# Optimization experiments

Hardware: AMD Instinct MI355X
Metric: run time of the kernel (lower is better)

## Reference

```python
import jax, jax.numpy as jnp
import numpy as np

B, T, D, H, DK, FF, V, L = 2, 1024, 768, 12, 64, 3072, 50257, 12


def setup_inputs() -> dict:
    key = jax.random.key(0)
    ks = jax.random.split(key, 9)
    s = 0.02  # matches nn.init.normal_(std=0.02)
    rn = lambda k, sh: jax.random.normal(k, sh, jnp.float32) * s
    return {
        "x": jax.random.randint(ks[0], (B, T), 0, V),
        "tok_emb": rn(ks[1], (V, D)),
        "pos_emb": rn(ks[2], (T, D)),
        "Wq": rn(ks[3], (L, D, D)), "bq": jnp.zeros((L, D), jnp.float32),
        "Wk": rn(ks[4], (L, D, D)), "bk": jnp.zeros((L, D), jnp.float32),
        "Wv": rn(ks[5], (L, D, D)), "bv": jnp.zeros((L, D), jnp.float32),
        "Wo": rn(ks[6], (L, D, D)), "bo": jnp.zeros((L, D), jnp.float32),
        "ln1_g": jnp.ones((L, D), jnp.float32), "ln1_b": jnp.zeros((L, D), jnp.float32),
        "ln2_g": jnp.ones((L, D), jnp.float32), "ln2_b": jnp.zeros((L, D), jnp.float32),
        "W1": rn(ks[7], (L, D, FF)), "b1": jnp.zeros((L, FF), jnp.float32),
        "W2": rn(ks[8], (L, FF, D)), "b2": jnp.zeros((L, D), jnp.float32),
        "lnf_g": jnp.ones((D,), jnp.float32), "lnf_b": jnp.zeros((D,), jnp.float32),
    }


def _ln(x, g, b, eps=1e-5):
    m = jnp.mean(x, axis=-1, keepdims=True)
    v = jnp.var(x, axis=-1, keepdims=True)  # biased var, like torch LayerNorm
    return (x - m) * jax.lax.rsqrt(v + eps) * g + b


def _forward(x, tok_emb, pos_emb, Wq, bq, Wk, bk, Wv, bv, Wo, bo,
             ln1_g, ln1_b, ln2_g, ln2_b, W1, b1, W2, b2, lnf_g, lnf_b):
    Bsz, Tn = x.shape
    h = tok_emb[x] + pos_emb[:Tn][None]  # [B,T,D]
    causal = jnp.tril(jnp.ones((Tn, Tn), dtype=bool))  # True = keep
    scale = 1.0 / np.sqrt(DK)

    def block(h, p):
        wq, bq_, wk, bk_, wv, bv_, wo, bo_, g1, be1, g2, be2, w1, bf1, w2, bf2 = p
        x2 = _ln(h, g1, be1)
        q = (x2 @ wq + bq_).reshape(Bsz, Tn, H, DK)
        k = (x2 @ wk + bk_).reshape(Bsz, Tn, H, DK)
        v = (x2 @ wv + bv_).reshape(Bsz, Tn, H, DK)
        scores = jnp.einsum("bqhd,bkhd->bhqk", q, k) * scale
        scores = jnp.where(causal, scores, -jnp.inf)
        attn = jax.nn.softmax(scores, axis=-1)  # dropout is identity in eval
        ctx = jnp.einsum("bhqk,bkhd->bqhd", attn, v).reshape(Bsz, Tn, D)
        h = h + ctx @ wo + bo_
        x2 = _ln(h, g2, be2)
        ff = jax.nn.gelu(x2 @ w1 + bf1, approximate=False) @ w2 + bf2  # exact GELU like F.gelu
        return h + ff, None

    params = (Wq, bq, Wk, bk, Wv, bv, Wo, bo, ln1_g, ln1_b, ln2_g, ln2_b, W1, b1, W2, b2)
    h, _ = jax.lax.scan(block, h, params)
    h = _ln(h, lnf_g, lnf_b)
    return h @ tok_emb.T  # tied lm_head, [B,T,V]


def reference(x, tok_emb, pos_emb, Wq, bq, Wk, bk, Wv, bv, Wo, bo,
              ln1_g, ln1_b, ln2_g, ln2_b, W1, b1, W2, b2, lnf_g, lnf_b):
    return _forward(x, tok_emb, pos_emb, Wq, bq, Wk, bk, Wv, bv, Wo, bo,
                    ln1_g, ln1_b, ln2_g, ln2_b, W1, b1, W2, b2, lnf_g, lnf_b)
```

## Files before the change

### kernel.cpp

```cpp
#include <hip/hip_runtime.h>
#include <cmath>

#define DI __device__ __forceinline__

typedef unsigned short u16;
typedef __bf16 bf16x8 __attribute__((ext_vector_type(8)));
typedef float f32x4 __attribute__((ext_vector_type(4)));

static constexpr int Bsz = 2, T = 1024, D = 768, H = 12, FF = 3072, V = 50257, L = 12;
static constexpr int M = Bsz * T;

DI u16 f2bf(float f) {
  unsigned u = __float_as_uint(f);
  u = (u + 0x7fffu + ((u >> 16) & 1u)) >> 16;
  return (u16)u;
}
DI float bf2f(u16 h) { return __uint_as_float(((unsigned)h) << 16); }

DI void gload_lds16(const void* g, void* l) {
  __builtin_amdgcn_global_load_lds((const __attribute__((address_space(1))) void*)g,
                                   (__attribute__((address_space(3))) void*)l, 16, 0, 0);
}

__launch_bounds__(256)
__global__ void transpose_cvt(const float* __restrict__ src, u16* __restrict__ dst, int R, int C) {
  __shared__ float tile[32][33];
  const int tx = threadIdx.x, ty = threadIdx.y;
  const int c0 = blockIdx.x * 32, r0 = blockIdx.y * 32;
  src += (size_t)blockIdx.z * R * C;
  dst += (size_t)blockIdx.z * R * C;
#pragma unroll
  for (int i = 0; i < 4; ++i)
    tile[ty + i * 8][tx] = src[(size_t)(r0 + ty + i * 8) * C + c0 + tx];
  __syncthreads();
#pragma unroll
  for (int i = 0; i < 4; ++i)
    dst[(size_t)(c0 + ty + i * 8) * R + r0 + tx] = f2bf(tile[tx][ty + i * 8]);
}

__global__ void convert_bf16(const float* __restrict__ src, u16* __restrict__ dst, long n4) {
  long i = (long)blockIdx.x * blockDim.x + threadIdx.x;
  long stride = (long)gridDim.x * blockDim.x;
  for (; i < n4; i += stride) {
    float4 f = ((const float4*)src)[i];
    ushort4 o;
    o.x = f2bf(f.x); o.y = f2bf(f.y); o.z = f2bf(f.z); o.w = f2bf(f.w);
    ((ushort4*)dst)[i] = o;
  }
}

__launch_bounds__(256)
__global__ void embed_kernel(const int* __restrict__ x, const float* __restrict__ tok,
                             const float* __restrict__ pos, float* __restrict__ h) {
  const int row = blockIdx.x, t = threadIdx.x;
  const int tt = row % T;
  const int id = x[row];
  float* o = h + (size_t)row * D;
  const float* te = tok + (size_t)id * D;
  const float* pe = pos + (size_t)tt * D;
  o[t] = te[t] + pe[t];
  o[t + 256] = te[t + 256] + pe[t + 256];
  o[t + 512] = te[t + 512] + pe[t + 512];
}

__launch_bounds__(256)
__global__ void layernorm_kernel(const float* __restrict__ in, const float* __restrict__ gw,
                                 const float* __restrict__ bw, u16* __restrict__ out) {
  const int row = blockIdx.x, t = threadIdx.x;
  const int lane = t & 63, wid = t >> 6;
  const float* x = in + (size_t)row * D;
  float v0 = x[t], v1 = x[t + 256], v2 = x[t + 512];
  float sum = v0 + v1 + v2;
  float sq = v0 * v0 + v1 * v1 + v2 * v2;
  for (int off = 1; off < 64; off <<= 1) {
    sum += __shfl_xor(sum, off);
    sq += __shfl_xor(sq, off);
  }
  __shared__ float ps[4], pq[4];
  if (lane == 0) { ps[wid] = sum; pq[wid] = sq; }
  __syncthreads();
  sum = ps[0] + ps[1] + ps[2] + ps[3];
  sq = pq[0] + pq[1] + pq[2] + pq[3];
  const float mean = sum * (1.0f / D);
  const float var = sq * (1.0f / D) - mean * mean;
  const float rstd = rsqrtf(var + 1e-5f);
  u16* o = out + (size_t)row * D;
  o[t] = f2bf((v0 - mean) * rstd * gw[t] + bw[t]);
  o[t + 256] = f2bf((v1 - mean) * rstd * gw[t + 256] + bw[t + 256]);
  o[t + 512] = f2bf((v2 - mean) * rstd * gw[t + 512] + bw[t + 512]);
}

template <int EPI, int BM, int BN, int BK>
DI void gemm_core(const u16* __restrict__ A, const u16* __restrict__ Bt,
                  const float* bias, float* outF, u16* outH, const float* resid,
                  int N, int K) {
  __shared__ u16 sA[BM * BK];
  __shared__ u16 sB[BN * BK];
  constexpr int FM = BM / 32, FN = BN / 32;
  constexpr int CPR = BK / 8;
  constexpr int KS = BK / 32;
  const int t = threadIdx.x;
  const int lane = t & 63, wid = t >> 6;
  const int m0 = blockIdx.x * BM, n0 = blockIdx.y * BN;

  f32x4 acc[FM][FN] = {};
  const int wr = (wid >> 1) * (BM / 2), wc = (wid & 1) * (BN / 2);
  const int rsel = lane & 15, ksel = lane >> 4;

  for (int k0 = 0; k0 < K; k0 += BK) {
#pragma unroll
    for (int i = 0; i < 2; ++i) {
      int c = t + i * 256;
      int row = c / CPR, ch = c % CPR;
      int g = ch ^ (row & (CPR - 1));
      gload_lds16(A + (size_t)(m0 + row) * K + k0 + g * 8, &sA[c * 8]);
    }
#pragma unroll
    for (int i = 0; i < 2; ++i) {
      int c = t + i * 256;
      int row = c / CPR, ch = c % CPR;
      int g = ch ^ (row & (CPR - 1));
      int nr = n0 + row;
      if (nr >= N) nr = N - 1;
      gload_lds16(Bt + (size_t)nr * K + k0 + g * 8, &sB[c * 8]);
    }
    __syncthreads();
#pragma unroll
    for (int ks = 0; ks < KS; ++ks) {
      bf16x8 af[FM], bfr[FN];
#pragma unroll
      for (int m = 0; m < FM; ++m) {
        int row = wr + m * 16 + rsel;
        int ch = (ksel + 4 * ks) ^ (row & (CPR - 1));
        af[m] = *(const bf16x8*)&sA[row * BK + ch * 8];
      }
#pragma unroll
      for (int n = 0; n < FN; ++n) {
        int row = wc + n * 16 + rsel;
        int ch = (ksel + 4 * ks) ^ (row & (CPR - 1));
        bfr[n] = *(const bf16x8*)&sB[row * BK + ch * 8];
      }
#pragma unroll
      for (int m = 0; m < FM; ++m)
#pragma unroll
        for (int n = 0; n < FN; ++n)
          acc[m][n] = __builtin_amdgcn_mfma_f32_16x16x32_bf16(af[m], bfr[n], acc[m][n], 0, 0, 0);
    }
    __syncthreads();
  }

  const int rq = lane >> 4;
#pragma unroll
  for (int m = 0; m < FM; ++m) {
#pragma unroll
    for (int n = 0; n < FN; ++n) {
      const int col = n0 + wc + n * 16 + rsel;
      if (col >= N) continue;
      const float bv = bias ? bias[col] : 0.0f;
#pragma unroll
      for (int i = 0; i < 4; ++i) {
        const int row = m0 + wr + m * 16 + rq * 4 + i;
        float v = acc[m][n][i] + bv;
        const size_t idx = (size_t)row * N + col;
        if (EPI == 0) {
          outH[idx] = f2bf(v);
        } else if (EPI == 1) {
          float ge = 0.5f * v * (1.0f + erff(v * 0.70710678118f));
          outH[idx] = f2bf(ge);
        } else if (EPI == 2) {
          outF[idx] = resid[idx] + v;
        } else {
          outF[idx] = v;
        }
      }
    }
  }
}

__launch_bounds__(256) __global__ void gemm_qkv(const u16* __restrict__ A, const u16* __restrict__ Bt,
                                                const float* b0, const float* b1, const float* b2,
                                                u16* out, long zsB, long zsOut) {
  const int z = blockIdx.z;
  gemm_core<0, 64, 64, 64>(A, Bt + (size_t)z * zsB, z == 0 ? b0 : (z == 1 ? b1 : b2),
                           nullptr, out + (size_t)z * zsOut, nullptr, D, D);
}
__launch_bounds__(256) __global__ void gemm_proj(const u16* __restrict__ A, const u16* __restrict__ Bt,
                                                 const float* bias, float* h) {
  gemm_core<2, 64, 64, 64>(A, Bt, bias, h, nullptr, h, D, D);
}
__launch_bounds__(256) __global__ void gemm_ff1(const u16* __restrict__ A, const u16* __restrict__ Bt,
                                                const float* bias, u16* out) {
  gemm_core<1, 128, 128, 32>(A, Bt, bias, nullptr, out, nullptr, FF, D);
}
__launch_bounds__(256) __global__ void gemm_ff2(const u16* __restrict__ A, const u16* __restrict__ Bt,
                                                const float* bias, float* h) {
  gemm_core<2, 64, 64, 64>(A, Bt, bias, h, nullptr, h, D, FF);
}
__launch_bounds__(256) __global__ void gemm_lm(const u16* __restrict__ A, const u16* __restrict__ Bt,
                                               float* out) {
  gemm_core<3, 128, 128, 32>(A, Bt, nullptr, out, nullptr, nullptr, V, D);
}

__launch_bounds__(256)
__global__ void attn_mfma(const u16* __restrict__ qbuf, const u16* __restrict__ kbuf,
                          const u16* __restrict__ vbuf, u16* __restrict__ ctx) {
  __shared__ u16 sK[64 * 64];
  __shared__ u16 sVT[64 * 72];
  __shared__ u16 sP[4][16 * 72];
  const int t = threadIdx.x, lane = t & 63, wid = t >> 6;
  const int l15 = lane & 15, g = lane >> 4;
  const int q0 = blockIdx.x * 64;
  const int bh = blockIdx.y;
  const int b = bh / H, hh = bh % H;
  const size_t rowbase = (size_t)b * T;
  u16* sPw = &sP[wid][0];

  const size_t qoff = (rowbase + q0 + wid * 16 + l15) * D + hh * 64 + g * 8;
  bf16x8 aQ0 = *(const bf16x8*)&qbuf[qoff];
  bf16x8 aQ1 = *(const bf16x8*)&qbuf[qoff + 32];

  float mr[4] = {-INFINITY, -INFINITY, -INFINITY, -INFINITY};
  float lr[4] = {0.f, 0.f, 0.f, 0.f};
  f32x4 o[4] = {};
  const int nt = blockIdx.x + 1;

  for (int kt = 0; kt < nt; ++kt) {
    __syncthreads();
#pragma unroll
    for (int i = 0; i < 2; ++i) {
      int c = t + i * 256;
      int row = c >> 3, ch = c & 7;
      gload_lds16(kbuf + (rowbase + kt * 64 + row) * D + hh * 64 + (size_t)(ch ^ (row & 7)) * 8,
                  &sK[c * 8]);
    }
#pragma unroll
    for (int i = 0; i < 2; ++i) {
      int key = t & 63, d0 = (t >> 6) * 8 + i * 32;
      bf16x8 v8 = *(const bf16x8*)&vbuf[(rowbase + kt * 64 + key) * D + hh * 64 + d0];
#pragma unroll
      for (int j = 0; j < 8; ++j) sVT[(d0 + j) * 72 + key] = ((u16*)&v8)[j];
    }
    __syncthreads();

    f32x4 s[4];
#pragma unroll
    for (int f = 0; f < 4; ++f) {
      const int krow = f * 16 + l15;
      bf16x8 bk0 = *(const bf16x8*)&sK[krow * 64 + ((g ^ (krow & 7)) * 8)];
      bf16x8 bk1 = *(const bf16x8*)&sK[krow * 64 + (((g + 4) ^ (krow & 7)) * 8)];
      f32x4 z = {};
      z = __builtin_amdgcn_mfma_f32_16x16x32_bf16(aQ0, bk0, z, 0, 0, 0);
      s[f] = __builtin_amdgcn_mfma_f32_16x16x32_bf16(aQ1, bk1, z, 0, 0, 0);
    }

    float p[4][4], scl[4];
#pragma unroll
    for (int i = 0; i < 4; ++i) {
      const int qrow = q0 + wid * 16 + g * 4 + i;
      const int kb = kt * 64 + l15;
      float v0 = (kb <= qrow) ? s[0][i] * 0.125f : -INFINITY;
      float v1 = (kb + 16 <= qrow) ? s[1][i] * 0.125f : -INFINITY;
      float v2 = (kb + 32 <= qrow) ? s[2][i] * 0.125f : -INFINITY;
      float v3 = (kb + 48 <= qrow) ? s[3][i] * 0.125f : -INFINITY;
      float mt = fmaxf(fmaxf(v0, v1), fmaxf(v2, v3));
#pragma unroll
      for (int off = 1; off < 16; off <<= 1) mt = fmaxf(mt, __shfl_xor(mt, off));
      const float mn = fmaxf(mr[i], mt);
      const float sc = __expf(mr[i] - mn);
      p[0][i] = __expf(v0 - mn); p[1][i] = __expf(v1 - mn);
      p[2][i] = __expf(v2 - mn); p[3][i] = __expf(v3 - mn);
      float rs = p[0][i] + p[1][i] + p[2][i] + p[3][i];
#pragma unroll
      for (int off = 1; off < 16; off <<= 1) rs += __shfl_xor(rs, off);
      lr[i] = lr[i] * sc + rs;
      mr[i] = mn;
      scl[i] = sc;
    }
#pragma unroll
    for (int n = 0; n < 4; ++n) {
      o[n][0] *= scl[0]; o[n][1] *= scl[1]; o[n][2] *= scl[2]; o[n][3] *= scl[3];
    }
#pragma unroll
    for (int f = 0; f < 4; ++f)
#pragma unroll
      for (int i = 0; i < 4; ++i)
        sPw[(g * 4 + i) * 72 + f * 16 + l15] = f2bf(p[f][i]);

#pragma unroll
    for (int kb = 0; kb < 2; ++kb) {
      bf16x8 pa = *(const bf16x8*)&sPw[l15 * 72 + kb * 32 + g * 8];
#pragma unroll
      for (int n = 0; n < 4; ++n) {
        bf16x8 bv = *(const bf16x8*)&sVT[(n * 16 + l15) * 72 + kb * 32 + g * 8];
        o[n] = __builtin_amdgcn_mfma_f32_16x16x32_bf16(pa, bv, o[n], 0, 0, 0);
      }
    }
  }

  float inv[4] = {1.0f / lr[0], 1.0f / lr[1], 1.0f / lr[2], 1.0f / lr[3]};
#pragma unroll
  for (int n = 0; n < 4; ++n)
#pragma unroll
    for (int i = 0; i < 4; ++i)
      ctx[(rowbase + q0 + wid * 16 + g * 4 + i) * D + hh * 64 + n * 16 + l15] =
          f2bf(o[n][i] * inv[i]);
}

extern "C" void kernel_launch(void* const* d_in, const int* in_sizes, int n_in,
                              void* d_out, int out_size, void* d_ws, size_t ws_size,
                              hipStream_t stream) {
  (void)in_sizes; (void)n_in; (void)out_size;
  const int* x = (const int*)d_in[0];
  const float* tok = (const float*)d_in[1];
  const float* pos = (const float*)d_in[2];
  const float* Wq = (const float*)d_in[3];
  const float* bq = (const float*)d_in[4];
  const float* Wk = (const float*)d_in[5];
  const float* bk = (const float*)d_in[6];
  const float* Wv = (const float*)d_in[7];
  const float* bv = (const float*)d_in[8];
  const float* Wo = (const float*)d_in[9];
  const float* bo = (const float*)d_in[10];
  const float* ln1_g = (const float*)d_in[11];
  const float* ln1_b = (const float*)d_in[12];
  const float* ln2_g = (const float*)d_in[13];
  const float* ln2_b = (const float*)d_in[14];
  const float* W1 = (const float*)d_in[15];
  const float* b1 = (const float*)d_in[16];
  const float* W2 = (const float*)d_in[17];
  const float* b2 = (const float*)d_in[18];
  const float* lnf_g = (const float*)d_in[19];
  const float* lnf_b = (const float*)d_in[20];

  char* ws = (char*)d_ws;
  size_t off = 0;
  auto alloc = [&](size_t bytes) {
    void* p = ws + off;
    off += (bytes + 255) & ~(size_t)255;
    return p;
  };
  u16* wqkvT = (u16*)alloc((size_t)3 * L * D * D * 2);
  u16* woT   = (u16*)alloc((size_t)L * D * D * 2);
  u16* w1T   = (u16*)alloc((size_t)L * D * FF * 2);
  u16* w2T   = (u16*)alloc((size_t)L * FF * D * 2);
  u16* tokT  = (u16*)alloc((size_t)V * D * 2);
  float* h   = (float*)alloc((size_t)M * D * 4);
  u16* x2    = (u16*)alloc((size_t)M * D * 2);
  u16* qkv   = (u16*)alloc((size_t)3 * M * D * 2);
  u16* ctx   = (u16*)alloc((size_t)M * D * 2);
  u16* ffb   = (u16*)alloc((size_t)M * FF * 2);
  u16* hf    = (u16*)alloc((size_t)M * D * 2);
  if (off > ws_size) return;

  const dim3 tb(32, 8);
  transpose_cvt<<<dim3(D / 32, D / 32, L), tb, 0, stream>>>(Wq, wqkvT + (size_t)0 * L * D * D, D, D);
  transpose_cvt<<<dim3(D / 32, D / 32, L), tb, 0, stream>>>(Wk, wqkvT + (size_t)1 * L * D * D, D, D);
  transpose_cvt<<<dim3(D / 32, D / 32, L), tb, 0, stream>>>(Wv, wqkvT + (size_t)2 * L * D * D, D, D);
  transpose_cvt<<<dim3(D / 32, D / 32, L), tb, 0, stream>>>(Wo, woT, D, D);
  transpose_cvt<<<dim3(FF / 32, D / 32, L), tb, 0, stream>>>(W1, w1T, D, FF);
  transpose_cvt<<<dim3(D / 32, FF / 32, L), tb, 0, stream>>>(W2, w2T, FF, D);
  convert_bf16<<<2048, 256, 0, stream>>>(tok, tokT, (long)V * D / 4);

  embed_kernel<<<M, 256, 0, stream>>>(x, tok, pos, h);

  for (int l = 0; l < L; ++l) {
    layernorm_kernel<<<M, 256, 0, stream>>>(h, ln1_g + (size_t)l * D, ln1_b + (size_t)l * D, x2);
    gemm_qkv<<<dim3(M / 64, D / 64, 3), 256, 0, stream>>>(
        x2, wqkvT + (size_t)l * D * D, bq + (size_t)l * D, bk + (size_t)l * D, bv + (size_t)l * D,
        qkv, (long)L * D * D, (long)M * D);
    attn_mfma<<<dim3(T / 64, Bsz * H), 256, 0, stream>>>(qkv, qkv + (size_t)M * D,
                                                         qkv + (size_t)2 * M * D, ctx);
    gemm_proj<<<dim3(M / 64, D / 64), 256, 0, stream>>>(ctx, woT + (size_t)l * D * D,
                                                        bo + (size_t)l * D, h);
    layernorm_kernel<<<M, 256, 0, stream>>>(h, ln2_g + (size_t)l * D, ln2_b + (size_t)l * D, x2);
    gemm_ff1<<<dim3(M / 128, FF / 128), 256, 0, stream>>>(x2, w1T + (size_t)l * D * FF,
                                                          b1 + (size_t)l * FF, ffb);
    gemm_ff2<<<dim3(M / 64, D / 64), 256, 0, stream>>>(ffb, w2T + (size_t)l * FF * D,
                                                       b2 + (size_t)l * D, h);
  }

  layernorm_kernel<<<M, 256, 0, stream>>>(h, lnf_g, lnf_b, hf);
  gemm_lm<<<dim3(M / 128, (V + 127) / 128), 256, 0, stream>>>(hf, tokT, (float*)d_out);
}
```

Baseline: 2.335 ms.

## Enlarge GEMM tiles, swizzle LM-head block order, reverse attention block order

GEMM tile sizes grow: QKV goes to 128x128, FF1 and the LM head move to BK=64, and the LM head uses 256x128 tiles. The LM-head grid is remapped so consecutive workgroups are spread across groups of eight, which is meant to improve L2 reuse of the weight and activation tiles. Attention now launches the longest causal query blocks first to reduce tail imbalance. Larger tiles cut load traffic per FLOP, but they use more LDS and registers and launch fewer blocks, which can reduce occupancy.

```diff
diff --git a/kernel.cpp b/kernel.cpp
--- a/kernel.cpp
+++ b/kernel.cpp
@@ -93,15 +93,16 @@
 template <int EPI, int BM, int BN, int BK>
 DI void gemm_core(const u16* __restrict__ A, const u16* __restrict__ Bt,
                   const float* bias, float* outF, u16* outH, const float* resid,
-                  int N, int K) {
+                  int N, int K, int m0, int n0) {
   __shared__ u16 sA[BM * BK];
   __shared__ u16 sB[BN * BK];
   constexpr int FM = BM / 32, FN = BN / 32;
   constexpr int CPR = BK / 8;
   constexpr int KS = BK / 32;
+  constexpr int AI = BM * BK / 8 / 256;
+  constexpr int BI = BN * BK / 8 / 256;
   const int t = threadIdx.x;
   const int lane = t & 63, wid = t >> 6;
-  const int m0 = blockIdx.x * BM, n0 = blockIdx.y * BN;
 
   f32x4 acc[FM][FN] = {};
   const int wr = (wid >> 1) * (BM / 2), wc = (wid & 1) * (BN / 2);
@@ -109,14 +110,14 @@
 
   for (int k0 = 0; k0 < K; k0 += BK) {
 #pragma unroll
-    for (int i = 0; i < 2; ++i) {
+    for (int i = 0; i < AI; ++i) {
       int c = t + i * 256;
       int row = c / CPR, ch = c % CPR;
       int g = ch ^ (row & (CPR - 1));
       gload_lds16(A + (size_t)(m0 + row) * K + k0 + g * 8, &sA[c * 8]);
     }
 #pragma unroll
-    for (int i = 0; i < 2; ++i) {
+    for (int i = 0; i < BI; ++i) {
       int c = t + i * 256;
       int row = c / CPR, ch = c % CPR;
       int g = ch ^ (row & (CPR - 1));
@@ -181,24 +182,31 @@
                                                 const float* b0, const float* b1, const float* b2,
                                                 u16* out, long zsB, long zsOut) {
   const int z = blockIdx.z;
-  gemm_core<0, 64, 64, 64>(A, Bt + (size_t)z * zsB, z == 0 ? b0 : (z == 1 ? b1 : b2),
-                           nullptr, out + (size_t)z * zsOut, nullptr, D, D);
+  gemm_core<0, 128, 128, 64>(A, Bt + (size_t)z * zsB, z == 0 ? b0 : (z == 1 ? b1 : b2),
+                             nullptr, out + (size_t)z * zsOut, nullptr, D, D,
+                             blockIdx.x * 128, blockIdx.y * 128);
 }
 __launch_bounds__(256) __global__ void gemm_proj(const u16* __restrict__ A, const u16* __restrict__ Bt,
                                                  const float* bias, float* h) {
-  gemm_core<2, 64, 64, 64>(A, Bt, bias, h, nullptr, h, D, D);
+  gemm_core<2, 64, 64, 64>(A, Bt, bias, h, nullptr, h, D, D, blockIdx.x * 64, blockIdx.y * 64);
 }
 __launch_bounds__(256) __global__ void gemm_ff1(const u16* __restrict__ A, const u16* __restrict__ Bt,
                                                 const float* bias, u16* out) {
-  gemm_core<1, 128, 128, 32>(A, Bt, bias, nullptr, out, nullptr, FF, D);
+  gemm_core<1, 128, 128, 64>(A, Bt, bias, nullptr, out, nullptr, FF, D,
+                             blockIdx.x * 128, blockIdx.y * 128);
 }
 __launch_bounds__(256) __global__ void gemm_ff2(const u16* __restrict__ A, const u16* __restrict__ Bt,
                                                 const float* bias, float* h) {
-  gemm_core<2, 64, 64, 64>(A, Bt, bias, h, nullptr, h, D, FF);
+  gemm_core<2, 64, 64, 64>(A, Bt, bias, h, nullptr, h, D, FF, blockIdx.x * 64, blockIdx.y * 64);
 }
 __launch_bounds__(256) __global__ void gemm_lm(const u16* __restrict__ A, const u16* __restrict__ Bt,
                                                float* out) {
-  gemm_core<3, 128, 128, 32>(A, Bt, nullptr, out, nullptr, nullptr, V, D);
+  const int flat = blockIdx.y * gridDim.x + blockIdx.x;
+  const int nwg = gridDim.x * gridDim.y;
+  const int cpx = nwg >> 3;
+  const int nf = (flat & 7) * cpx + (flat >> 3);
+  const int m0 = (nf % 8) * 256, n0 = (nf / 8) * 128;
+  gemm_core<3, 256, 128, 64>(A, Bt, nullptr, out, nullptr, nullptr, V, D, m0, n0);
 }
 
 __launch_bounds__(256)
@@ -209,7 +217,8 @@
   __shared__ u16 sP[4][16 * 72];
   const int t = threadIdx.x, lane = t & 63, wid = t >> 6;
   const int l15 = lane & 15, g = lane >> 4;
-  const int q0 = blockIdx.x * 64;
+  const int qc = gridDim.x - 1 - blockIdx.x;
+  const int q0 = qc * 64;
   const int bh = blockIdx.y;
   const int b = bh / H, hh = bh % H;
   const size_t rowbase = (size_t)b * T;
@@ -222,7 +231,7 @@
   float mr[4] = {-INFINITY, -INFINITY, -INFINITY, -INFINITY};
   float lr[4] = {0.f, 0.f, 0.f, 0.f};
   f32x4 o[4] = {};
-  const int nt = blockIdx.x + 1;
+  const int nt = qc + 1;
 
   for (int kt = 0; kt < nt; ++kt) {
     __syncthreads();
@@ -365,7 +374,7 @@
 
   for (int l = 0; l < L; ++l) {
     layernorm_kernel<<<M, 256, 0, stream>>>(h, ln1_g + (size_t)l * D, ln1_b + (size_t)l * D, x2);
-    gemm_qkv<<<dim3(M / 64, D / 64, 3), 256, 0, stream>>>(
+    gemm_qkv<<<dim3(M / 128, D / 128, 3), 256, 0, stream>>>(
         x2, wqkvT + (size_t)l * D * D, bq + (size_t)l * D, bk + (size_t)l * D, bv + (size_t)l * D,
         qkv, (long)L * D * D, (long)M * D);
     attn_mfma<<<dim3(T / 64, Bsz * H), 256, 0, stream>>>(qkv, qkv + (size_t)M * D,
@@ -380,5 +389,5 @@
   }
 
   layernorm_kernel<<<M, 256, 0, stream>>>(h, lnf_g, lnf_b, hf);
-  gemm_lm<<<dim3(M / 128, (V + 127) / 128), 256, 0, stream>>>(hf, tokT, (float*)d_out);
-}
+  gemm_lm<<<dim3(M / 256, (V + 127) / 128), 256, 0, stream>>>(hf, tokT, (float*)d_out);
+}
```

After: 2.483 ms. +6.3%, slower.
